# Optimization experiments

Hardware: AMD Instinct MI355X
Metric: run time of the kernel (lower is better)

Reference implementation:

```python
import jax, jax.numpy as jnp
import numpy as np

N, E, F, L, G, C = 100000, 1600000, 128, 3, 512, 40
BN_EPS = 1e-5


def gcn_conv(x, src, dst, W, b, n_nodes):
    # PyG GCNConv: linear transform, symmetric normalization with self-loops,
    # scatter-add aggregation, then bias.
    xw = x @ W                                   # [N, H]
    deg = jnp.zeros((n_nodes,), x.dtype).at[dst].add(1.0) + 1.0  # +1 self-loop
    dinv = jax.lax.rsqrt(deg)                    # D^{-1/2}
    norm = dinv[src] * dinv[dst]                 # [E]
    msg = xw[src] * norm[:, None]                # gather + scale, [E, H]
    agg = jnp.zeros_like(xw).at[dst].add(msg)    # scatter-add to destinations
    agg = agg + xw * (dinv * dinv)[:, None]      # self-loop contribution
    return agg + b


def setup_inputs() -> dict:
    key = jax.random.key(0)
    ks = jax.random.split(key, 6)
    x = jax.random.normal(ks[0], (N, F), dtype=jnp.float32)
    edge_index = jax.random.randint(ks[1], (2, E), 0, N, dtype=jnp.int64)
    batch = jnp.sort(jax.random.randint(ks[2], (N,), 0, G, dtype=jnp.int64))
    conv_w = jax.random.normal(ks[3], (L, F, F), dtype=jnp.float32) * 0.05
    conv_b = jnp.zeros((L, F), dtype=jnp.float32)
    bn_gamma = jnp.ones((L, F), dtype=jnp.float32)
    bn_beta = jnp.zeros((L, F), dtype=jnp.float32)
    bn_mean = jnp.zeros((L, F), dtype=jnp.float32)
    bn_var = jnp.ones((L, F), dtype=jnp.float32)
    lin_w = jax.random.normal(ks[4], (F, C), dtype=jnp.float32) * 0.05
    lin_b = jnp.zeros((C,), dtype=jnp.float32)
    return {"x": x, "edge_index": edge_index, "batch": batch,
            "conv_w": conv_w, "conv_b": conv_b,
            "bn_gamma": bn_gamma, "bn_beta": bn_beta,
            "bn_mean": bn_mean, "bn_var": bn_var,
            "lin_w": lin_w, "lin_b": lin_b}


def reference(x, edge_index, batch, conv_w, conv_b, bn_gamma, bn_beta,
              bn_mean, bn_var, lin_w, lin_b):
    src, dst = edge_index[0], edge_index[1]
    h = x
    # layers 0..L-2: conv -> BN(eval) -> ReLU (dropout is identity in eval)
    for i in range(L - 1):
        h = gcn_conv(h, src, dst, conv_w[i], conv_b[i], N)
        h = (h - bn_mean[i]) * (bn_gamma[i] * jax.lax.rsqrt(bn_var[i] + BN_EPS)) + bn_beta[i]
        h = jax.nn.relu(h)
    # last conv (no BN/ReLU)
    h = gcn_conv(h, src, dst, conv_w[L - 1], conv_b[L - 1], N)
    # global_mean_pool over graphs
    sums = jnp.zeros((G, F), h.dtype).at[batch].add(h)
    counts = jnp.zeros((G,), h.dtype).at[batch].add(1.0)
    pooled = sums / jnp.maximum(counts, 1.0)[:, None]   # [G, F]
    return pooled @ lin_w + lin_b                        # [G, C]
```

## Files before the change

### kernel.cpp

```cpp
#include <hip/hip_runtime.h>

#define Nn 100000
#define Ee 1600000
#define Ff 128
#define Gg 512
#define Cc 40
#define NCH 2048
#define CH  49

__global__ void prep_scales_k(const float* __restrict__ conv_b,
                              const float* __restrict__ gamma,
                              const float* __restrict__ beta,
                              const float* __restrict__ mean,
                              const float* __restrict__ var,
                              float* __restrict__ sc, float* __restrict__ sh)
{
    int i = blockIdx.x * blockDim.x + threadIdx.x;
    if (i >= 3 * Ff) return;
    float b = conv_b[i];
    if (i < 2 * Ff) {
        float s = gamma[i] * rsqrtf(var[i] + 1e-5f);
        sc[i] = s;
        sh[i] = (b - mean[i]) * s + beta[i];
    } else {
        sc[i] = 1.0f;
        sh[i] = b;
    }
}

__global__ void count_edges_k(const int* __restrict__ dst, int* __restrict__ deg)
{
    int e = blockIdx.x * 256 + threadIdx.x;
    if (e < Ee) atomicAdd(&deg[dst[e]], 1);
}

__global__ void chunk_sum_k(const int* __restrict__ deg, int* __restrict__ csum)
{
    int t = blockIdx.x * 256 + threadIdx.x;
    if (t >= NCH) return;
    int i0 = t * CH, i1 = min(i0 + CH, Nn);
    int s = 0;
    for (int i = i0; i < i1; ++i) s += deg[i];
    csum[t] = s;
}

__global__ void scan_chunks_k(const int* __restrict__ csum, int* __restrict__ coff)
{
    __shared__ int tot[256];
    int t = threadIdx.x;
    int v[8]; int s = 0;
    #pragma unroll
    for (int j = 0; j < 8; ++j) { v[j] = csum[t * 8 + j]; s += v[j]; }
    tot[t] = s;
    __syncthreads();
    for (int d = 1; d < 256; d <<= 1) {
        int x = (t >= d) ? tot[t - d] : 0;
        __syncthreads();
        tot[t] += x;
        __syncthreads();
    }
    int base = tot[t] - s;
    #pragma unroll
    for (int j = 0; j < 8; ++j) { coff[t * 8 + j] = base; base += v[j]; }
}

__global__ void write_offsets_k(const int* __restrict__ deg, const int* __restrict__ coff,
                                int* __restrict__ off, float* __restrict__ dinv)
{
    int t = blockIdx.x * 256 + threadIdx.x;
    if (t >= NCH) return;
    int i0 = t * CH, i1 = min(i0 + CH, Nn);
    int run = coff[t];
    for (int i = i0; i < i1; ++i) {
        off[i] = run;
        int d = deg[i];
        run += d;
        dinv[i] = rsqrtf((float)d + 1.0f);
    }
    if (t == 0) off[Nn] = Ee;
}

__global__ void fill_csr_k(const int* __restrict__ src, const int* __restrict__ dst,
                           const int* __restrict__ off, int* __restrict__ cur,
                           int* __restrict__ csrc)
{
    int e = blockIdx.x * 256 + threadIdx.x;
    if (e < Ee) {
        int d = dst[e];
        int p = off[d] + atomicAdd(&cur[d], 1);
        csrc[p] = src[e];
    }
}

__global__ __launch_bounds__(256) void gemm_scale_k(
    const float* __restrict__ A, const float* __restrict__ W,
    const float* __restrict__ dinv, float* __restrict__ Y, int n)
{
    const int tid  = threadIdx.x;
    const int half = __builtin_amdgcn_readfirstlane(tid >> 7);
    const int cb   = half * 64;
    const int r    = blockIdx.x * 128 + (tid & 127);
    const int rr   = min(r, n - 1);
    const float4* Ap = (const float4*)(A + ((size_t)rr << 7));
    const float*  Wp = W + cb;

    float acc[64];
    #pragma unroll
    for (int c = 0; c < 64; ++c) acc[c] = 0.f;

    for (int kc = 0; kc < 4; ++kc) {
        float4 a[8];
        #pragma unroll
        for (int i = 0; i < 8; ++i) a[i] = Ap[kc * 8 + i];
        const float* af = reinterpret_cast<const float*>(a);
        #pragma unroll
        for (int kk = 0; kk < 32; ++kk) {
            const float av = af[kk];
            const float* wr = Wp + (kc * 32 + kk) * Ff;
            #pragma unroll
            for (int c = 0; c < 64; ++c)
                acc[c] = fmaf(av, wr[c], acc[c]);
        }
    }

    if (r < n) {
        const float di = dinv[r];
        float* yp = Y + ((size_t)r << 7) + cb;
        #pragma unroll
        for (int c = 0; c < 64; c += 4)
            *(float4*)(yp + c) = make_float4(acc[c] * di, acc[c + 1] * di,
                                             acc[c + 2] * di, acc[c + 3] * di);
    }
}

__global__ __launch_bounds__(256) void aggregate_half_k(
    const float* __restrict__ Y, const int* __restrict__ off,
    const int* __restrict__ srcs, const float* __restrict__ dinv,
    const float* __restrict__ sc, const float* __restrict__ sh,
    const int* __restrict__ batch,
    float* __restrict__ H, float* __restrict__ pool,
    int cb, int dorelu, int n)
{
    const int wid  = threadIdx.x >> 6;
    const int lane = threadIdx.x & 63;
    const int node = blockIdx.x * 4 + wid;
    if (node >= n) return;
    const int beg = off[node], end = off[node + 1];
    const float* Yc = Y + cb + lane;

    float acc  = Yc[node << 7];
    float acc2 = 0.f;

    for (int e = beg; e < end; e += 64) {
        const int nb = min(64, end - e);
        int sidx = (lane < nb) ? srcs[e + lane] : 0;
        int j = 0;
        for (; j + 8 <= nb; j += 8) {
            int s0 = __shfl(sidx, j + 0);
            int s1 = __shfl(sidx, j + 1);
            int s2 = __shfl(sidx, j + 2);
            int s3 = __shfl(sidx, j + 3);
            int s4 = __shfl(sidx, j + 4);
            int s5 = __shfl(sidx, j + 5);
            int s6 = __shfl(sidx, j + 6);
            int s7 = __shfl(sidx, j + 7);
            float v0 = Yc[s0 << 7];
            float v1 = Yc[s1 << 7];
            float v2 = Yc[s2 << 7];
            float v3 = Yc[s3 << 7];
            float v4 = Yc[s4 << 7];
            float v5 = Yc[s5 << 7];
            float v6 = Yc[s6 << 7];
            float v7 = Yc[s7 << 7];
            acc += v0; acc2 += v1; acc += v2; acc2 += v3;
            acc += v4; acc2 += v5; acc += v6; acc2 += v7;
        }
        for (; j < nb; ++j) {
            int s = __shfl(sidx, j);
            acc += Yc[s << 7];
        }
    }
    acc += acc2;

    const float di = dinv[node];
    float o = acc * di * sc[cb + lane] + sh[cb + lane];
    if (dorelu) o = fmaxf(o, 0.f);
    if (pool) {
        atomicAdd(&pool[(batch[node] << 7) + cb + lane], o);
    } else {
        H[(node << 7) + cb + lane] = o;
    }
}

__global__ __launch_bounds__(128) void out_k(
    const float* __restrict__ pool, const int* __restrict__ batch,
    const float* __restrict__ lw, const float* __restrict__ lb,
    float* __restrict__ out)
{
    int g = blockIdx.x, f = threadIdx.x;
    int lo = 0, hi = Nn;
    while (lo < hi) { int m = (lo + hi) >> 1; if (batch[m] < g) lo = m + 1; else hi = m; }
    int start = lo;
    hi = Nn;
    while (lo < hi) { int m = (lo + hi) >> 1; if (batch[m] < g + 1) lo = m + 1; else hi = m; }
    int cnt = lo - start;
    float invc = 1.0f / (float)max(cnt, 1);

    __shared__ float pooled[Ff];
    pooled[f] = pool[(g << 7) + f] * invc;
    __syncthreads();
    if (f < Cc) {
        float o = lb[f];
        #pragma unroll 8
        for (int k = 0; k < Ff; ++k) o += pooled[k] * lw[k * Cc + f];
        out[g * Cc + f] = o;
    }
}

extern "C" void kernel_launch(void* const* d_in, const int* in_sizes, int n_in,
                              void* d_out, int out_size, void* d_ws, size_t ws_size,
                              hipStream_t stream)
{
    const float* x      = (const float*)d_in[0];
    const int*   ei     = (const int*)d_in[1];
    const int*   batch  = (const int*)d_in[2];
    const float* conv_w = (const float*)d_in[3];
    const float* conv_b = (const float*)d_in[4];
    const float* gamma  = (const float*)d_in[5];
    const float* beta   = (const float*)d_in[6];
    const float* mean   = (const float*)d_in[7];
    const float* var    = (const float*)d_in[8];
    const float* lw     = (const float*)d_in[9];
    const float* lb     = (const float*)d_in[10];
    float* out = (float*)d_out;

    const int* srcp = ei;
    const int* dstp = ei + Ee;

    float* h    = (float*)d_ws;
    float* y    = h + (size_t)Nn * Ff;
    float* dinv = y + (size_t)Nn * Ff;
    float* sc   = dinv + Nn;
    float* sh   = sc + 3 * Ff;
    int*   deg  = (int*)(sh + 3 * Ff);
    int*   cur  = deg + Nn;
    float* pool = (float*)(cur + Nn);
    int*   off  = (int*)(pool + Gg * Ff);
    int*   csrc = off + (Nn + 1);
    int*   csum = csrc + Ee;
    int*   coff = csum + NCH;

    hipMemsetAsync(deg, 0, (2 * (size_t)Nn + Gg * Ff) * sizeof(int), stream);

    prep_scales_k<<<2, 256, 0, stream>>>(conv_b, gamma, beta, mean, var, sc, sh);
    count_edges_k<<<Ee / 256, 256, 0, stream>>>(dstp, deg);
    chunk_sum_k<<<NCH / 256, 256, 0, stream>>>(deg, csum);
    scan_chunks_k<<<1, 256, 0, stream>>>(csum, coff);
    write_offsets_k<<<NCH / 256, 256, 0, stream>>>(deg, coff, off, dinv);
    fill_csr_k<<<Ee / 256, 256, 0, stream>>>(srcp, dstp, off, cur, csrc);

    const int gemm_grid = (Nn + 127) / 128;
    const int agg_grid  = (Nn + 3) / 4;
    for (int l = 0; l < 3; ++l) {
        const float* in = (l == 0) ? x : h;
        gemm_scale_k<<<gemm_grid, 256, 0, stream>>>(in, conv_w + (size_t)l * Ff * Ff,
                                                    dinv, y, Nn);
        float* poolp = (l == 2) ? pool : nullptr;
        for (int p = 0; p < 2; ++p)
            aggregate_half_k<<<agg_grid, 256, 0, stream>>>(
                y, off, csrc, dinv, sc + l * Ff, sh + l * Ff, batch,
                h, poolp, p * 64, (l < 2) ? 1 : 0, Nn);
    }
    out_k<<<Gg, 128, 0, stream>>>(pool, batch, lw, lb, out);
}
```

Before: 912.1 us.

## Build CSR via bucketed two-pass sort and aggregate full rows per wave

Replaces per-node atomic degree counting and the scattered CSR fill with a two-level bucket sort. Edges are first binned into 64-node buckets using padded counters and staged with packed local ids, then one block per bucket computes offsets and dinv and scatters into the CSR in shared memory. The aggregation is also merged into a single pass where each lane handles two features via float2, replacing two half-width launches that each re-read the index list. This cuts global atomic contention and halves index traffic, at the cost of reusing the h buffer as staging space and a more complex preprocessing pipeline.

```diff
diff --git a/kernel.cpp b/kernel.cpp
--- a/kernel.cpp
+++ b/kernel.cpp
@@ -5,8 +5,8 @@
 #define Ff 128
 #define Gg 512
 #define Cc 40
-#define NCH 2048
-#define CH  49
+#define NB 1563
+#define PAD 32
 
 __global__ void prep_scales_k(const float* __restrict__ conv_b,
                               const float* __restrict__ gamma,
@@ -28,29 +28,24 @@
     }
 }
 
-__global__ void count_edges_k(const int* __restrict__ dst, int* __restrict__ deg)
+__global__ void bucket_count_k(const int* __restrict__ dst, int* __restrict__ bcnt)
 {
     int e = blockIdx.x * 256 + threadIdx.x;
-    if (e < Ee) atomicAdd(&deg[dst[e]], 1);
-}
-
-__global__ void chunk_sum_k(const int* __restrict__ deg, int* __restrict__ csum)
-{
-    int t = blockIdx.x * 256 + threadIdx.x;
-    if (t >= NCH) return;
-    int i0 = t * CH, i1 = min(i0 + CH, Nn);
-    int s = 0;
-    for (int i = i0; i < i1; ++i) s += deg[i];
-    csum[t] = s;
-}
-
-__global__ void scan_chunks_k(const int* __restrict__ csum, int* __restrict__ coff)
+    if (e < Ee) atomicAdd(&bcnt[(dst[e] >> 6) * PAD], 1);
+}
+
+__global__ void scan_buckets_k(const int* __restrict__ bcnt, int* __restrict__ bktOff,
+                               int* __restrict__ off)
 {
     __shared__ int tot[256];
     int t = threadIdx.x;
-    int v[8]; int s = 0;
+    int v[7]; int s = 0;
     #pragma unroll
-    for (int j = 0; j < 8; ++j) { v[j] = csum[t * 8 + j]; s += v[j]; }
+    for (int j = 0; j < 7; ++j) {
+        int idx = t * 7 + j;
+        int val = (idx < NB) ? bcnt[idx * PAD] : 0;
+        v[j] = val; s += val;
+    }
     tot[t] = s;
     __syncthreads();
     for (int d = 1; d < 256; d <<= 1) {
@@ -61,34 +56,59 @@
     }
     int base = tot[t] - s;
     #pragma unroll
-    for (int j = 0; j < 8; ++j) { coff[t * 8 + j] = base; base += v[j]; }
-}
-
-__global__ void write_offsets_k(const int* __restrict__ deg, const int* __restrict__ coff,
-                                int* __restrict__ off, float* __restrict__ dinv)
-{
-    int t = blockIdx.x * 256 + threadIdx.x;
-    if (t >= NCH) return;
-    int i0 = t * CH, i1 = min(i0 + CH, Nn);
-    int run = coff[t];
-    for (int i = i0; i < i1; ++i) {
-        off[i] = run;
-        int d = deg[i];
-        run += d;
-        dinv[i] = rsqrtf((float)d + 1.0f);
-    }
-    if (t == 0) off[Nn] = Ee;
-}
-
-__global__ void fill_csr_k(const int* __restrict__ src, const int* __restrict__ dst,
-                           const int* __restrict__ off, int* __restrict__ cur,
-                           int* __restrict__ csrc)
+    for (int j = 0; j < 7; ++j) {
+        int idx = t * 7 + j;
+        if (idx < NB) bktOff[idx] = base;
+        base += v[j];
+    }
+    if (t == 255) { bktOff[NB] = base; off[Nn] = base; }
+}
+
+__global__ void bucket_fill_k(const int* __restrict__ src, const int* __restrict__ dst,
+                              const int* __restrict__ bktOff, int* __restrict__ bcur,
+                              int* __restrict__ staged)
 {
     int e = blockIdx.x * 256 + threadIdx.x;
     if (e < Ee) {
         int d = dst[e];
-        int p = off[d] + atomicAdd(&cur[d], 1);
-        csrc[p] = src[e];
+        int b = d >> 6;
+        int p = atomicAdd(&bcur[b * PAD], 1);
+        staged[bktOff[b] + p] = src[e] | ((d & 63) << 17);
+    }
+}
+
+__global__ __launch_bounds__(256) void bucket_scatter_k(
+    const int* __restrict__ staged, const int* __restrict__ bktOff,
+    int* __restrict__ off, float* __restrict__ dinv, int* __restrict__ csrc)
+{
+    __shared__ int cl[64], ol[64], cu[64];
+    const int b = blockIdx.x, tid = threadIdx.x;
+    const int base = bktOff[b], base2 = bktOff[b + 1];
+    if (tid < 64) cl[tid] = 0;
+    __syncthreads();
+    for (int i = base + tid; i < base2; i += 256)
+        atomicAdd(&cl[staged[i] >> 17], 1);
+    __syncthreads();
+    if (tid == 0) {
+        int r = 0;
+        #pragma unroll
+        for (int l = 0; l < 64; ++l) { ol[l] = r; r += cl[l]; }
+    }
+    __syncthreads();
+    if (tid < 64) {
+        int node = b * 64 + tid;
+        if (node < Nn) {
+            off[node]  = base + ol[tid];
+            dinv[node] = rsqrtf((float)cl[tid] + 1.0f);
+        }
+        cu[tid] = 0;
+    }
+    __syncthreads();
+    for (int i = base + tid; i < base2; i += 256) {
+        int w = staged[i];
+        int l = w >> 17;
+        int pos = atomicAdd(&cu[l], 1);
+        csrc[base + ol[l] + pos] = w & 0x1FFFF;
     }
 }
 
@@ -133,62 +153,58 @@
     }
 }
 
-__global__ __launch_bounds__(256) void aggregate_half_k(
+__global__ __launch_bounds__(256) void aggregate_k(
     const float* __restrict__ Y, const int* __restrict__ off,
     const int* __restrict__ srcs, const float* __restrict__ dinv,
     const float* __restrict__ sc, const float* __restrict__ sh,
     const int* __restrict__ batch,
-    float* __restrict__ H, float* __restrict__ pool,
-    int cb, int dorelu, int n)
-{
-    const int wid  = threadIdx.x >> 6;
-    const int lane = threadIdx.x & 63;
-    const int node = blockIdx.x * 4 + wid;
+    float* __restrict__ H, float* __restrict__ pool, int dorelu, int n)
+{
+    int wid  = threadIdx.x >> 6;
+    int lane = threadIdx.x & 63;
+    int node = blockIdx.x * 4 + wid;
     if (node >= n) return;
-    const int beg = off[node], end = off[node + 1];
-    const float* Yc = Y + cb + lane;
-
-    float acc  = Yc[node << 7];
-    float acc2 = 0.f;
+    int beg = off[node], end = off[node + 1];
+    int c = lane * 2;
+
+    float2 self = *(const float2*)(Y + ((size_t)node << 7) + c);
+    float ax = self.x, ay = self.y;
+    float bx = 0.f,    by = 0.f;
 
     for (int e = beg; e < end; e += 64) {
-        const int nb = min(64, end - e);
+        int nb = min(64, end - e);
         int sidx = (lane < nb) ? srcs[e + lane] : 0;
         int j = 0;
-        for (; j + 8 <= nb; j += 8) {
-            int s0 = __shfl(sidx, j + 0);
+        for (; j + 4 <= nb; j += 4) {
+            int s0 = __shfl(sidx, j);
             int s1 = __shfl(sidx, j + 1);
             int s2 = __shfl(sidx, j + 2);
             int s3 = __shfl(sidx, j + 3);
-            int s4 = __shfl(sidx, j + 4);
-            int s5 = __shfl(sidx, j + 5);
-            int s6 = __shfl(sidx, j + 6);
-            int s7 = __shfl(sidx, j + 7);
-            float v0 = Yc[s0 << 7];
-            float v1 = Yc[s1 << 7];
-            float v2 = Yc[s2 << 7];
-            float v3 = Yc[s3 << 7];
-            float v4 = Yc[s4 << 7];
-            float v5 = Yc[s5 << 7];
-            float v6 = Yc[s6 << 7];
-            float v7 = Yc[s7 << 7];
-            acc += v0; acc2 += v1; acc += v2; acc2 += v3;
-            acc += v4; acc2 += v5; acc += v6; acc2 += v7;
+            float2 v0 = *(const float2*)(Y + ((size_t)s0 << 7) + c);
+            float2 v1 = *(const float2*)(Y + ((size_t)s1 << 7) + c);
+            float2 v2 = *(const float2*)(Y + ((size_t)s2 << 7) + c);
+            float2 v3 = *(const float2*)(Y + ((size_t)s3 << 7) + c);
+            ax += v0.x; ay += v0.y; bx += v1.x; by += v1.y;
+            ax += v2.x; ay += v2.y; bx += v3.x; by += v3.y;
         }
         for (; j < nb; ++j) {
-            int s = __shfl(sidx, j);
-            acc += Yc[s << 7];
-        }
-    }
-    acc += acc2;
-
-    const float di = dinv[node];
-    float o = acc * di * sc[cb + lane] + sh[cb + lane];
-    if (dorelu) o = fmaxf(o, 0.f);
+            int s0 = __shfl(sidx, j);
+            float2 v0 = *(const float2*)(Y + ((size_t)s0 << 7) + c);
+            ax += v0.x; ay += v0.y;
+        }
+    }
+    float di = dinv[node];
+    float2 scv = *(const float2*)(sc + c);
+    float2 shv = *(const float2*)(sh + c);
+    float ox = (ax + bx) * di * scv.x + shv.x;
+    float oy = (ay + by) * di * scv.y + shv.y;
+    if (dorelu) { ox = fmaxf(ox, 0.f); oy = fmaxf(oy, 0.f); }
     if (pool) {
-        atomicAdd(&pool[(batch[node] << 7) + cb + lane], o);
+        float* pp = pool + ((size_t)batch[node] << 7) + c;
+        atomicAdd(pp,     ox);
+        atomicAdd(pp + 1, oy);
     } else {
-        H[(node << 7) + cb + lane] = o;
+        *(float2*)(H + ((size_t)node << 7) + c) = make_float2(ox, oy);
     }
 }
 
@@ -237,27 +253,26 @@
     const int* srcp = ei;
     const int* dstp = ei + Ee;
 
-    float* h    = (float*)d_ws;
-    float* y    = h + (size_t)Nn * Ff;
-    float* dinv = y + (size_t)Nn * Ff;
-    float* sc   = dinv + Nn;
-    float* sh   = sc + 3 * Ff;
-    int*   deg  = (int*)(sh + 3 * Ff);
-    int*   cur  = deg + Nn;
-    float* pool = (float*)(cur + Nn);
-    int*   off  = (int*)(pool + Gg * Ff);
-    int*   csrc = off + (Nn + 1);
-    int*   csum = csrc + Ee;
-    int*   coff = csum + NCH;
-
-    hipMemsetAsync(deg, 0, (2 * (size_t)Nn + Gg * Ff) * sizeof(int), stream);
+    float* h      = (float*)d_ws;
+    float* y      = h + (size_t)Nn * Ff;
+    float* dinv   = y + (size_t)Nn * Ff;
+    float* sc     = dinv + Nn;
+    float* sh     = sc + 3 * Ff;
+    int*   bcnt   = (int*)(sh + 3 * Ff);
+    int*   bcur   = bcnt + NB * PAD;
+    float* pool   = (float*)(bcur + NB * PAD);
+    int*   off    = (int*)(pool + Gg * Ff);
+    int*   csrc   = off + (Nn + 1);
+    int*   bktOff = csrc + Ee;
+    int*   staged = (int*)h;
+
+    hipMemsetAsync(bcnt, 0, (size_t)(2 * NB * PAD + Gg * Ff) * sizeof(int), stream);
 
     prep_scales_k<<<2, 256, 0, stream>>>(conv_b, gamma, beta, mean, var, sc, sh);
-    count_edges_k<<<Ee / 256, 256, 0, stream>>>(dstp, deg);
-    chunk_sum_k<<<NCH / 256, 256, 0, stream>>>(deg, csum);
-    scan_chunks_k<<<1, 256, 0, stream>>>(csum, coff);
-    write_offsets_k<<<NCH / 256, 256, 0, stream>>>(deg, coff, off, dinv);
-    fill_csr_k<<<Ee / 256, 256, 0, stream>>>(srcp, dstp, off, cur, csrc);
+    bucket_count_k<<<Ee / 256, 256, 0, stream>>>(dstp, bcnt);
+    scan_buckets_k<<<1, 256, 0, stream>>>(bcnt, bktOff, off);
+    bucket_fill_k<<<Ee / 256, 256, 0, stream>>>(srcp, dstp, bktOff, bcur, staged);
+    bucket_scatter_k<<<NB, 256, 0, stream>>>(staged, bktOff, off, dinv, csrc);
 
     const int gemm_grid = (Nn + 127) / 128;
     const int agg_grid  = (Nn + 3) / 4;
@@ -265,11 +280,9 @@
         const float* in = (l == 0) ? x : h;
         gemm_scale_k<<<gemm_grid, 256, 0, stream>>>(in, conv_w + (size_t)l * Ff * Ff,
                                                     dinv, y, Nn);
-        float* poolp = (l == 2) ? pool : nullptr;
-        for (int p = 0; p < 2; ++p)
-            aggregate_half_k<<<agg_grid, 256, 0, stream>>>(
-                y, off, csrc, dinv, sc + l * Ff, sh + l * Ff, batch,
-                h, poolp, p * 64, (l < 2) ? 1 : 0, Nn);
+        aggregate_k<<<agg_grid, 256, 0, stream>>>(
+            y, off, csrc, dinv, sc + l * Ff, sh + l * Ff, batch,
+            h, (l == 2) ? pool : nullptr, (l < 2) ? 1 : 0, Nn);
     }
     out_k<<<Gg, 128, 0, stream>>>(pool, batch, lw, lb, out);
 }
```

Measured after the change: 871.9 us. -4.4%, faster.
